# Kernel tuning notes

Measured on AMD Instinct MI355X. Metric: run time of the kernel, lower is better.

Reference implementation:

```python
import jax, jax.numpy as jnp
import numpy as np

NUM_EMBEDDINGS = 512
EMBEDDING_DIM = 100
COMMITMENT_COST = 0.25


def setup_inputs() -> dict:
    key = jax.random.key(0)
    k1, k2 = jax.random.split(key)
    inputs = jax.random.normal(k1, (64, 64, 64, EMBEDDING_DIM), dtype=jnp.float32)
    # nn.Embedding weight init: uniform(-1/num_embeddings, 1/num_embeddings)
    lim = 1.0 / NUM_EMBEDDINGS
    embedding = jax.random.uniform(k2, (NUM_EMBEDDINGS, EMBEDDING_DIM),
                                   dtype=jnp.float32, minval=-lim, maxval=lim)
    return {"inputs": inputs, "embedding": embedding}


def reference(inputs, embedding):
    d = inputs.shape[-1]
    flat = inputs.reshape(-1, d)                                  # [N, d]
    # squared L2 distances to each codebook entry: [N, K]
    distances = (jnp.sum(flat ** 2, axis=1, keepdims=True)
                 + jnp.sum(embedding ** 2, axis=1)
                 - 2.0 * flat @ embedding.T)
    encoding_indices = jnp.argmin(distances, axis=1)              # [N]
    quantized = embedding[encoding_indices].reshape(inputs.shape)
    commitment_loss = COMMITMENT_COST * jnp.mean(
        (jax.lax.stop_gradient(quantized) - inputs) ** 2)
    quantization_loss = jnp.mean(
        (quantized - jax.lax.stop_gradient(inputs)) ** 2)
    # straight-through estimator
    quantized_st = inputs + jax.lax.stop_gradient(quantized - inputs)
    return quantized_st, quantization_loss, commitment_loss
```

## Files before the change

kernel.cpp:

```cpp
#include <hip/hip_runtime.h>
#include <hip/hip_bf16.h>
#include <cfloat>


#define N_ROWS (64 * 64 * 64)
#define D 100
#define KCODES 512
#define CB_OFF 4096
#define E2_OFF 16

typedef __attribute__((ext_vector_type(8))) short short8;
typedef __attribute__((ext_vector_type(4))) float f32x4;

__device__ __forceinline__ unsigned short f2bf(float f) {
    union { float f; unsigned u; } v; v.f = f;
    unsigned r = v.u + 0x7FFF + ((v.u >> 16) & 1);
    return (unsigned short)(r >> 16);
}
__device__ __forceinline__ unsigned pk2(float a, float b) {
    union { __hip_bfloat162 h; unsigned u; } c;
    c.h = __float22bfloat162_rn(make_float2(a, b));
    return c.u;
}
__device__ __forceinline__ short8 pack8(const float4& a, const float4& b) {
    union { unsigned u[4]; short8 v; } r;
    r.u[0] = pk2(a.x, a.y); r.u[1] = pk2(a.z, a.w);
    r.u[2] = pk2(b.x, b.y); r.u[3] = pk2(b.z, b.w);
    return r.v;
}

__global__ __launch_bounds__(64) void vq_init(const float* __restrict__ emb,
                                              float* __restrict__ ws) {
    const int code = blockIdx.x, l = threadIdx.x;
    const float* e = emb + code * D;
    if (code == 0 && l == 0) ws[0] = 0.0f;
    float a = e[l];
    float b = (l < D - 64) ? e[64 + l] : 0.0f;
    float p = fmaf(a, a, b * b);
#pragma unroll
    for (int off = 32; off; off >>= 1) p += __shfl_xor(p, off);
    if (l == 0) ws[E2_OFF + code] = p;

    if (l < 16) {
        const int s = l >> 2, q = l & 3;
        short8 v;
#pragma unroll
        for (int j = 0; j < 8; ++j) {
            int k = s * 32 + q * 8 + j;
            v[j] = (k < D) ? (short)f2bf(e[k]) : (short)0;
        }
        const int chunk = code >> 5, ci = code & 31;
        const int tt = ci >> 4, lr = ci & 15;
        unsigned short* cb = (unsigned short*)((char*)ws + CB_OFF);
        *(short8*)(cb + chunk * 4096 + ((s * 2 + tt) * 64 + q * 16 + lr) * 8) = v;
    }
}

__global__ __launch_bounds__(256, 2) void vq_main(const float* __restrict__ x,
                                                  const float* __restrict__ emb,
                                                  float* __restrict__ ws,
                                                  float* __restrict__ out) {
    __shared__ uint4  bbuf[2][512];
    __shared__ float  e2s[KCODES];
    __shared__ int    widx[256];
    __shared__ float  wsum[4];

    const int tid = threadIdx.x, wave = tid >> 6, lane = tid & 63;
    const int quad = lane >> 4, lr = lane & 15;
    const long brow = (long)blockIdx.x * 256;
    const long wrow = brow + wave * 64;

    float4 av[4][7];
#pragma unroll
    for (int m = 0; m < 4; ++m) {
        const float* xr = x + (wrow + m * 16 + lr) * D + quad * 8;
        av[m][0] = *(const float4*)(xr);
        av[m][1] = *(const float4*)(xr + 4);
        av[m][2] = *(const float4*)(xr + 32);
        av[m][3] = *(const float4*)(xr + 36);
        av[m][4] = *(const float4*)(xr + 64);
        av[m][5] = *(const float4*)(xr + 68);
        av[m][6] = *(const float4*)(x + (wrow + m * 16 + lr) * D + 96);
    }

    const uint4* __restrict__ cbg = (const uint4*)((const char*)ws + CB_OFF);
    uint4 st0 = cbg[wave * 128 + lane];
    uint4 st1 = cbg[wave * 128 + 64 + lane];
    const float* __restrict__ e2g = ws + E2_OFF;
    e2s[tid]       = e2g[tid];
    e2s[256 + tid] = e2g[256 + tid];

    short8 A[4][4];
    float  xnorm[4];
#pragma unroll
    for (int m = 0; m < 4; ++m) {
        float4 z = av[m][6];
        if (quad != 0) z = make_float4(0.f, 0.f, 0.f, 0.f);
        float nrm = 0.f;
#pragma unroll
        for (int i = 0; i < 6; ++i) {
            float4 f = av[m][i];
            nrm = fmaf(f.x, f.x, nrm); nrm = fmaf(f.y, f.y, nrm);
            nrm = fmaf(f.z, f.z, nrm); nrm = fmaf(f.w, f.w, nrm);
        }
        nrm = fmaf(z.x, z.x, nrm); nrm = fmaf(z.y, z.y, nrm);
        nrm = fmaf(z.z, z.z, nrm); nrm = fmaf(z.w, z.w, nrm);
        A[m][0] = pack8(av[m][0], av[m][1]);
        A[m][1] = pack8(av[m][2], av[m][3]);
        A[m][2] = pack8(av[m][4], av[m][5]);
        A[m][3] = pack8(z, make_float4(0.f, 0.f, 0.f, 0.f));
        nrm += __shfl_xor(nrm, 16);
        nrm += __shfl_xor(nrm, 32);
        xnorm[m] = nrm;
    }

    bbuf[0][wave * 128 + lane]      = st0;
    bbuf[0][wave * 128 + 64 + lane] = st1;
    __syncthreads();

    float    runmin[4][4];
    unsigned runidx[4][4];
#pragma unroll
    for (int m = 0; m < 4; ++m)
#pragma unroll
        for (int r = 0; r < 4; ++r) { runmin[m][r] = FLT_MAX; runidx[m][r] = 0; }

    for (int c = 0; c < 16; ++c) {
        const int p = c & 1;
        uint4 n0, n1;
        if (c < 15) {
            n0 = cbg[(c + 1) * 512 + wave * 128 + lane];
            n1 = cbg[(c + 1) * 512 + wave * 128 + 64 + lane];
        }

        const short8* __restrict__ bl = (const short8*)&bbuf[p][0];
        short8 B[2][4];
#pragma unroll
        for (int s = 0; s < 4; ++s) {
            B[0][s] = bl[(s * 2 + 0) * 64 + lane];
            B[1][s] = bl[(s * 2 + 1) * 64 + lane];
        }
        float e2v0 = e2s[c * 32 + lr];
        float e2v1 = e2s[c * 32 + 16 + lr];

        f32x4 acc[4][2];
#pragma unroll
        for (int m = 0; m < 4; ++m) {
            acc[m][0] = (f32x4){0.f, 0.f, 0.f, 0.f};
            acc[m][1] = (f32x4){0.f, 0.f, 0.f, 0.f};
        }
#pragma unroll
        for (int s = 0; s < 4; ++s)
#pragma unroll
            for (int m = 0; m < 4; ++m) {
                acc[m][0] = __builtin_amdgcn_mfma_f32_16x16x32_bf16(A[m][s], B[0][s], acc[m][0], 0, 0, 0);
                acc[m][1] = __builtin_amdgcn_mfma_f32_16x16x32_bf16(A[m][s], B[1][s], acc[m][1], 0, 0, 0);
            }

#pragma unroll
        for (int m = 0; m < 4; ++m)
#pragma unroll
            for (int tt = 0; tt < 2; ++tt) {
                float e2v = tt ? e2v1 : e2v0;
                unsigned code = c * 32 + tt * 16 + lr;
#pragma unroll
                for (int r = 0; r < 4; ++r) {
                    float sc = fmaf(-2.0f, acc[m][tt][r], e2v);
                    if (sc < runmin[m][r]) { runmin[m][r] = sc; runidx[m][r] = code; }
                }
            }

        if (c < 15) {
            bbuf[p ^ 1][wave * 128 + lane]      = n0;
            bbuf[p ^ 1][wave * 128 + 64 + lane] = n1;
        }
        __syncthreads();
    }

    float lsum = 0.0f;
#pragma unroll
    for (int m = 0; m < 4; ++m)
#pragma unroll
        for (int r = 0; r < 4; ++r) {
            float    s = runmin[m][r];
            unsigned i = runidx[m][r];
#pragma unroll
            for (int off = 8; off >= 1; off >>= 1) {
                float    os = __shfl_xor(s, off);
                unsigned oi = (unsigned)__shfl_xor((int)i, off);
                if (os < s || (os == s && oi < i)) { s = os; i = oi; }
            }
            if (lr == quad * 4 + r) {
                lsum += xnorm[m] + s;
                widx[wave * 64 + m * 16 + quad * 4 + r] = (int)i;
            }
        }
#pragma unroll
    for (int off = 32; off >= 1; off >>= 1) lsum += __shfl_xor(lsum, off);
    if (lane == 0) wsum[wave] = lsum;
    __syncthreads();
    if (tid == 0) atomicAdd(ws, wsum[0] + wsum[1] + wsum[2] + wsum[3]);

    const float4* __restrict__ ef = (const float4*)emb;
    float4* __restrict__ og = (float4*)(out + brow * D);
#pragma unroll
    for (int i = 0; i < 25; i += 5) {
        float4 q[5];
        int    gi[5];
#pragma unroll
        for (int u = 0; u < 5; ++u) {
            int g = (i + u) * 256 + tid;
            int row = g / 25;
            int c4  = g - row * 25;
            gi[u] = g;
            q[u]  = ef[(long)widx[row] * 25 + c4];
        }
#pragma unroll
        for (int u = 0; u < 5; ++u) og[gi[u]] = q[u];
    }
}

__global__ void vq_final(const float* __restrict__ ws, float* __restrict__ out) {
    float mse = ws[0] / (float)((long)N_ROWS * D);
    out[(long)N_ROWS * D]     = mse;
    out[(long)N_ROWS * D + 1] = 0.25f * mse;
}

extern "C" void kernel_launch(void* const* d_in, const int* in_sizes, int n_in,
                              void* d_out, int out_size, void* d_ws, size_t ws_size,
                              hipStream_t stream) {
    const float* x   = (const float*)d_in[0];
    const float* emb = (const float*)d_in[1];
    float* out = (float*)d_out;
    float* ws  = (float*)d_ws;

    vq_init<<<KCODES, 64, 0, stream>>>(emb, ws);
    vq_main<<<N_ROWS / 256, 256, 0, stream>>>(x, emb, ws, out);
    vq_final<<<1, 1, 0, stream>>>(ws, out);
}
```

Measured before the change: 233.8 us.

## Read codebook fragments directly from global memory, drop LDS staging and barriers

Removes the double-buffered LDS staging of the bf16 codebook and the e2 norms. Each wave now loads its B fragments and e2 values straight from global memory, which should hit L2/L1 since every block reads the same 100KB. This eliminates the per-chunk __syncthreads and the LDS traffic, and the freed registers and LDS allow the occupancy hint to rise from 2 to 3 blocks per SIMD. The risk is higher global-load latency sitting on the MFMA critical path, since there is no explicit prefetch of the next chunk.

```diff
diff --git a/kernel.cpp b/kernel.cpp
--- a/kernel.cpp
+++ b/kernel.cpp
@@ -56,12 +56,10 @@
     }
 }
 
-__global__ __launch_bounds__(256, 2) void vq_main(const float* __restrict__ x,
+__global__ __launch_bounds__(256, 3) void vq_main(const float* __restrict__ x,
                                                   const float* __restrict__ emb,
                                                   float* __restrict__ ws,
                                                   float* __restrict__ out) {
-    __shared__ uint4  bbuf[2][512];
-    __shared__ float  e2s[KCODES];
     __shared__ int    widx[256];
     __shared__ float  wsum[4];
 
@@ -83,13 +81,6 @@
         av[m][6] = *(const float4*)(x + (wrow + m * 16 + lr) * D + 96);
     }
 
-    const uint4* __restrict__ cbg = (const uint4*)((const char*)ws + CB_OFF);
-    uint4 st0 = cbg[wave * 128 + lane];
-    uint4 st1 = cbg[wave * 128 + 64 + lane];
-    const float* __restrict__ e2g = ws + E2_OFF;
-    e2s[tid]       = e2g[tid];
-    e2s[256 + tid] = e2g[256 + tid];
-
     short8 A[4][4];
     float  xnorm[4];
 #pragma unroll
@@ -114,9 +105,8 @@
         xnorm[m] = nrm;
     }
 
-    bbuf[0][wave * 128 + lane]      = st0;
-    bbuf[0][wave * 128 + 64 + lane] = st1;
-    __syncthreads();
+    const short8* __restrict__ bgall = (const short8*)((const char*)ws + CB_OFF);
+    const float*  __restrict__ e2g   = ws + E2_OFF;
 
     float    runmin[4][4];
     unsigned runidx[4][4];
@@ -126,55 +116,32 @@
         for (int r = 0; r < 4; ++r) { runmin[m][r] = FLT_MAX; runidx[m][r] = 0; }
 
     for (int c = 0; c < 16; ++c) {
-        const int p = c & 1;
-        uint4 n0, n1;
-        if (c < 15) {
-            n0 = cbg[(c + 1) * 512 + wave * 128 + lane];
-            n1 = cbg[(c + 1) * 512 + wave * 128 + 64 + lane];
-        }
-
-        const short8* __restrict__ bl = (const short8*)&bbuf[p][0];
-        short8 B[2][4];
-#pragma unroll
-        for (int s = 0; s < 4; ++s) {
-            B[0][s] = bl[(s * 2 + 0) * 64 + lane];
-            B[1][s] = bl[(s * 2 + 1) * 64 + lane];
-        }
-        float e2v0 = e2s[c * 32 + lr];
-        float e2v1 = e2s[c * 32 + 16 + lr];
-
-        f32x4 acc[4][2];
-#pragma unroll
-        for (int m = 0; m < 4; ++m) {
-            acc[m][0] = (f32x4){0.f, 0.f, 0.f, 0.f};
-            acc[m][1] = (f32x4){0.f, 0.f, 0.f, 0.f};
-        }
-#pragma unroll
-        for (int s = 0; s < 4; ++s)
-#pragma unroll
-            for (int m = 0; m < 4; ++m) {
-                acc[m][0] = __builtin_amdgcn_mfma_f32_16x16x32_bf16(A[m][s], B[0][s], acc[m][0], 0, 0, 0);
-                acc[m][1] = __builtin_amdgcn_mfma_f32_16x16x32_bf16(A[m][s], B[1][s], acc[m][1], 0, 0, 0);
-            }
-
-#pragma unroll
-        for (int m = 0; m < 4; ++m)
-#pragma unroll
-            for (int tt = 0; tt < 2; ++tt) {
-                float e2v = tt ? e2v1 : e2v0;
-                unsigned code = c * 32 + tt * 16 + lr;
+        const short8* __restrict__ bg = bgall + c * 512;
+#pragma unroll
+        for (int tt = 0; tt < 2; ++tt) {
+            short8 B[4];
+#pragma unroll
+            for (int s = 0; s < 4; ++s) B[s] = bg[(s * 2 + tt) * 64 + lane];
+            float e2v = e2g[c * 32 + tt * 16 + lr];
+
+            f32x4 acc[4];
+#pragma unroll
+            for (int m = 0; m < 4; ++m) acc[m] = (f32x4){0.f, 0.f, 0.f, 0.f};
+#pragma unroll
+            for (int s = 0; s < 4; ++s)
+#pragma unroll
+                for (int m = 0; m < 4; ++m)
+                    acc[m] = __builtin_amdgcn_mfma_f32_16x16x32_bf16(A[m][s], B[s], acc[m], 0, 0, 0);
+
+            const unsigned code = c * 32 + tt * 16 + lr;
+#pragma unroll
+            for (int m = 0; m < 4; ++m)
 #pragma unroll
                 for (int r = 0; r < 4; ++r) {
-                    float sc = fmaf(-2.0f, acc[m][tt][r], e2v);
+                    float sc = fmaf(-2.0f, acc[m][r], e2v);
                     if (sc < runmin[m][r]) { runmin[m][r] = sc; runidx[m][r] = code; }
                 }
-            }
-
-        if (c < 15) {
-            bbuf[p ^ 1][wave * 128 + lane]      = n0;
-            bbuf[p ^ 1][wave * 128 + 64 + lane] = n1;
-        }
-        __syncthreads();
+        }
     }
 
     float lsum = 0.0f;
```

After: 242.2 us. +3.6%, slower.
